# Performance work log

Measured on AMD Instinct MI355X. Metric: run time of the kernel, lower is better.

The kernel has to match this reference:

```python
import jax, jax.numpy as jnp
import numpy as np

B, H, W, C = 4, 256, 256, 16
NT = 9


def _rot2(a):
    c, s = np.cos(a), np.sin(a)
    return np.array([[c, -s], [s, c]])


def _aff(m2):
    p = np.eye(3)
    p[:2, :2] = m2
    return p


def _t(tx, ty):
    p = np.eye(3)
    p[0, 2] = tx
    p[1, 2] = ty
    return p


def _refl(direction):
    # reflection across line through origin spanned by `direction`
    v = np.asarray(direction, dtype=np.float64)
    m2 = 2.0 * np.outer(v, v) / np.dot(v, v) - np.eye(2)
    return _aff(m2)


def _get_transforms(t0, t1, t2):
    L = np.eye(3)
    L[:2, 0] = t1
    L[:2, 1] = t2
    L[:2, 2] = t0
    rot = lambda n: _aff(_rot2(2.0 * np.pi / n))
    e = np.eye(3)
    r2 = _t(.5, .5) @ rot(2) @ _t(-.5, -.5)
    r3 = _t(.5, .5) @ rot(3) @ _t(-.5, -.5)
    r4 = _t(.5, .5) @ rot(4) @ _t(-.5, -.5)
    r6 = _t(.5, .5) @ rot(6) @ _t(-.5, -.5)
    f_p = _t(0, .5) @ np.diag([1.0, -1.0, 1.0]) @ _t(0, -.5)
    f_c = np.array([[0.0, 1, 0], [1, 0, 0], [0, 0, 1]])
    f_l = _t(.5, .5) @ _refl(_rot2(5 * np.pi / 6) @ np.array([1.0, 0.0])) @ _t(-.5, -.5)
    f_s = _t(.5, .5) @ _refl(_rot2(np.pi / 3) @ np.array([1.0, 0.0])) @ _t(-.5, -.5)
    Ts = np.stack([e, r2, r3, r4, r6, f_p, f_c, f_l, f_s])
    Ts = L[None] @ Ts @ np.linalg.inv(L)[None]
    Ts = np.linalg.inv(Ts)
    Ts = Ts / Ts[:, 2:3, 2:3]  # normalize so last entry is 1
    return Ts.reshape(NT, 9)[:, :8].astype(np.float32)  # TF flat transform params


def setup_inputs() -> dict:
    key = jax.random.key(0)
    inputs = jax.random.normal(key, (B, H, W, C), dtype=jnp.float32)
    transforms = jnp.asarray(_get_transforms((0.0, 0.0), (float(H), 0.0), (0.0, float(W))))
    return {"inputs": inputs, "transforms": transforms}


def _warp_nearest(img, flat):
    # TF image_projective_transform_v2 semantics with NEAREST interpolation,
    # constant (zero) fill. flat maps OUTPUT (x,y) -> INPUT (x,y).
    b, h, w, c = img.shape
    yy, xx = jnp.meshgrid(jnp.arange(h, dtype=jnp.float32),
                          jnp.arange(w, dtype=jnp.float32), indexing="ij")
    a0, a1, a2, a3, a4, a5, a6, a7 = [flat[i] for i in range(8)]
    k = a6 * xx + a7 * yy + 1.0
    xi = jnp.round((a0 * xx + a1 * yy + a2) / k).astype(jnp.int32)
    yi = jnp.round((a3 * xx + a4 * yy + a5) / k).astype(jnp.int32)
    valid = (xi >= 0) & (xi < w) & (yi >= 0) & (yi < h)
    xi = jnp.clip(xi, 0, w - 1)
    yi = jnp.clip(yi, 0, h - 1)
    out = img[:, yi, xi, :]  # [b,h,w,c] gather
    return jnp.where(valid[None, :, :, None], out, 0.0)


def _forward(inputs, transforms):
    b, h, w, c = inputs.shape
    nt = transforms.shape[0]
    # warp the input by each of the nt group transforms: [nt,b,h,w,c]
    yw = jax.vmap(lambda m: _warp_nearest(inputs, m))(transforms)
    x = jnp.broadcast_to(inputs[None], yw.shape)
    x = jnp.transpose(x, (0, 1, 4, 2, 3))   # [nt,b,c,h,w]
    yw = jnp.transpose(yw, (0, 1, 4, 2, 3))
    # circular normalized cross-correlation via FFT, per channel image
    fx = jnp.fft.rfft2(x)
    fy = jnp.fft.rfft2(yw)
    corr = jnp.fft.irfft2(fx * jnp.conj(fy), s=(h, w))  # [nt,b,c,h,w]
    nx = jnp.linalg.norm(x.reshape(nt, b, c, -1), axis=-1)[..., None, None]
    ny = jnp.linalg.norm(yw.reshape(nt, b, c, -1), axis=-1)[..., None, None]
    corr = corr / (nx * ny + 1e-12)
    out = corr.mean(axis=2)                  # mean over channels -> [nt,b,h,w]
    return jnp.transpose(out, (1, 2, 3, 0))  # channels_last [b,h,w,nt]


def reference(inputs, transforms):
    return _forward(inputs, transforms)
```

## Files before the change

kernel.cpp:

```cpp
#include <hip/hip_runtime.h>
#include <hip/hip_fp16.h>

#define Bn  4
#define Hn  256
#define Wn  256
#define Cn  16
#define NTn 9
#define HWn (Hn*Wn)
#define KF  129
#define KGP 136
#define SRL 266
#define PI_F 3.14159265358979323846f

__device__ __forceinline__ int swz(int i) { return i ^ ((i >> 4) & 15); }

__device__ __forceinline__ float2 cmul(float2 a, float2 b) {
  float2 r = make_float2(a.x, a.x) * b;
  return r + make_float2(-a.y, a.y) * make_float2(b.y, b.x);
}

template<bool INV>
__device__ __forceinline__ void radix4(float2& x0, float2& x1, float2& x2, float2& x3) {
  float2 y0 = x0 + x2;
  float2 y1 = x0 - x2;
  float2 y2 = x1 + x3;
  float2 y3 = x1 - x3;
  float2 j3 = INV ? make_float2(-y3.y, y3.x) : make_float2(y3.y, -y3.x);
  x0 = y0 + y2;
  x2 = y0 - y2;
  x1 = y1 + j3;
  x3 = y1 - j3;
}

struct Tw { float2 a1,a2,a3,b1,b2,b3,c1,c2,c3; };

template<bool INV>
__device__ __forceinline__ Tw make_tw(int lane) {
  const float sgn = INV ? 2.0f * PI_F : -2.0f * PI_F;
  Tw t; float sw, cw;
  __sincosf(sgn * (float)lane / 256.0f, &sw, &cw);
  t.a1 = make_float2(cw, sw); t.a2 = cmul(t.a1, t.a1); t.a3 = cmul(t.a2, t.a1);
  __sincosf(sgn * (float)(lane & 15) / 64.0f, &sw, &cw);
  t.b1 = make_float2(cw, sw); t.b2 = cmul(t.b1, t.b1); t.b3 = cmul(t.b2, t.b1);
  __sincosf(sgn * (float)(lane & 3) / 16.0f, &sw, &cw);
  t.c1 = make_float2(cw, sw); t.c2 = cmul(t.c1, t.c1); t.c3 = cmul(t.c2, t.c1);
  return t;
}

template<bool INV, int NF>
__device__ __forceinline__ void fft256_n(float2 (*v)[4], float2 (*s)[SRL],
                                         int lane, const Tw& t) {
#pragma unroll
  for (int f = 0; f < NF; ++f) {
    radix4<INV>(v[f][0], v[f][1], v[f][2], v[f][3]);
    v[f][1] = cmul(v[f][1], t.a1); v[f][2] = cmul(v[f][2], t.a2); v[f][3] = cmul(v[f][3], t.a3);
#pragma unroll
    for (int a = 0; a < 4; ++a) s[f][swz(lane + (a << 6))] = v[f][a];
  }
  { int base = (lane >> 4) * 64 + (lane & 15);
#pragma unroll
    for (int f = 0; f < NF; ++f)
#pragma unroll
      for (int a = 0; a < 4; ++a) v[f][a] = s[f][swz(base + (a << 4))];
  }
#pragma unroll
  for (int f = 0; f < NF; ++f) {
    radix4<INV>(v[f][0], v[f][1], v[f][2], v[f][3]);
    v[f][1] = cmul(v[f][1], t.b1); v[f][2] = cmul(v[f][2], t.b2); v[f][3] = cmul(v[f][3], t.b3);
    int base = (lane >> 4) * 64 + (lane & 15);
#pragma unroll
    for (int a = 0; a < 4; ++a) s[f][swz(base + (a << 4))] = v[f][a];
  }
  { int base = (lane >> 4) * 64 + ((lane >> 2) & 3) * 16 + (lane & 3);
#pragma unroll
    for (int f = 0; f < NF; ++f)
#pragma unroll
      for (int a = 0; a < 4; ++a) v[f][a] = s[f][swz(base + (a << 2))];
  }
#pragma unroll
  for (int f = 0; f < NF; ++f) {
    radix4<INV>(v[f][0], v[f][1], v[f][2], v[f][3]);
    v[f][1] = cmul(v[f][1], t.c1); v[f][2] = cmul(v[f][2], t.c2); v[f][3] = cmul(v[f][3], t.c3);
    int base = (lane & ~3) * 4 + (lane & 3);
#pragma unroll
    for (int a = 0; a < 4; ++a) s[f][swz(base + (a << 2))] = v[f][a];
  }
  { int base = lane * 4;
#pragma unroll
    for (int f = 0; f < NF; ++f)
#pragma unroll
      for (int a = 0; a < 4; ++a) v[f][a] = s[f][swz(base + a)];
  }
  int dr = ((lane & 3) << 4) + (((lane >> 2) & 3) << 2) + (lane >> 4);
#pragma unroll
  for (int f = 0; f < NF; ++f) {
    radix4<INV>(v[f][0], v[f][1], v[f][2], v[f][3]);
#pragma unroll
    for (int a = 0; a < 4; ++a) s[f][swz(dr + (a << 6))] = v[f][a];
  }
}

__device__ __forceinline__ int warp_id2(float a0, float a2, float a3, float a5,
                                        float a6, float p1, float p4, float p7,
                                        bool affine, int col) {
#pragma clang fp contract(off)
  float x = (float)col;
  float xf = (a0 * x + p1) + a2;
  float yf = (a3 * x + p4) + a5;
  if (!affine) {
    float kk = (a6 * x + p7) + 1.0f;
    xf = xf / kk;
    yf = yf / kk;
  }
  float xr = rintf(xf), yr = rintf(yf);
  bool valid = (xr >= 0.f) && (xr < 256.f) && (yr >= 0.f) && (yr < 256.f);
  return valid ? ((int)yr * Wn + (int)xr) : -1;
}

__global__ __launch_bounds__(256) void k_yrow(const float* __restrict__ inp,
                                              const float* __restrict__ T,
                                              __half2* __restrict__ Yh,
                                              float* __restrict__ part) {
  __shared__ float2 sb[4][4][SRL];
  __shared__ float4 redw[4];
  int tid = threadIdx.x, w = tid >> 6, lane = tid & 63;
  Tw t = make_tw<false>(lane);
  int chunk = blockIdx.x & 15, cg = (blockIdx.x >> 4) & 3, tb = blockIdx.x >> 6;
  int b = tb & 3, tt = tb >> 2;
  int i0 = chunk << 4;
  const float4* ib = (const float4*)(inp + (size_t)b * HWn * Cn);
  float a0, a1, a2, a3, a4, a5, a6, a7;
  { const float* a = T + tt * 8;
    a0=a[0]; a1=a[1]; a2=a[2]; a3=a[3]; a4=a[4]; a5=a[5]; a6=a[6]; a7=a[7]; }
  const bool affine = (fabsf(a6) + fabsf(a7)) * 255.0f < 2.9e-8f;
  float4 nyacc = make_float4(0.f, 0.f, 0.f, 0.f);

  auto store_half = [&](int h) {
    int ii = tid & 7, kq = tid >> 3;
    int w2 = ii >> 1, odd = ii & 1;
#pragma unroll
    for (int p = 0; p < 5; ++p) {
      int k = p * 32 + kq;
      if (k <= 128) {
        int kc = (256 - k) & 255;
#pragma unroll
        for (int cc = 0; cc < 4; ++cc) {
          float2 Z  = sb[w2][cc][swz(k)];
          float2 Zc = sb[w2][cc][swz(kc)];
          float2 F = odd ? make_float2(0.5f * (Z.y + Zc.y), 0.5f * (Zc.x - Z.x))
                         : make_float2(0.5f * (Z.x + Zc.x), 0.5f * (Z.y - Zc.y));
          Yh[((size_t)(tb * Cn + cg * 4 + cc) * KF + k) * Hn + i0 + h * 8 + ii] =
              __float22half2_rn(F);
        }
      }
    }
  };

  {
    int r0 = i0 + 2 * w;
    float yA = (float)r0, yB = (float)(r0 + 1);
    float p1A = a1 * yA, p4A = a4 * yA, p7A = a7 * yA;
    float p1B = a1 * yB, p4B = a4 * yB, p7B = a7 * yB;
    float4 g0[4], g1[4];
#pragma unroll
    for (int q = 0; q < 4; ++q) {
      int col = lane + (q << 6);
      int id0 = warp_id2(a0, a2, a3, a5, a6, p1A, p4A, p7A, affine, col);
      int id1 = warp_id2(a0, a2, a3, a5, a6, p1B, p4B, p7B, affine, col);
      g0[q] = (id0 >= 0) ? ib[(size_t)id0 * 4 + cg] : make_float4(0.f,0.f,0.f,0.f);
      g1[q] = (id1 >= 0) ? ib[(size_t)id1 * 4 + cg] : make_float4(0.f,0.f,0.f,0.f);
      nyacc += g0[q] * g0[q] + g1[q] * g1[q];
    }
    float2 v[4][4];
#pragma unroll
    for (int q = 0; q < 4; ++q) {
      v[0][q] = make_float2(g0[q].x, g1[q].x);
      v[1][q] = make_float2(g0[q].y, g1[q].y);
      v[2][q] = make_float2(g0[q].z, g1[q].z);
      v[3][q] = make_float2(g0[q].w, g1[q].w);
    }
    fft256_n<false, 4>(v, sb[w], lane, t);
  }
  __syncthreads();

  float4 G0[4], G1[4];
  {
    int r1 = i0 + 8 + 2 * w;
    float yA = (float)r1, yB = (float)(r1 + 1);
    float p1A = a1 * yA, p4A = a4 * yA, p7A = a7 * yA;
    float p1B = a1 * yB, p4B = a4 * yB, p7B = a7 * yB;
#pragma unroll
    for (int q = 0; q < 4; ++q) {
      int col = lane + (q << 6);
      int id0 = warp_id2(a0, a2, a3, a5, a6, p1A, p4A, p7A, affine, col);
      int id1 = warp_id2(a0, a2, a3, a5, a6, p1B, p4B, p7B, affine, col);
      G0[q] = (id0 >= 0) ? ib[(size_t)id0 * 4 + cg] : make_float4(0.f,0.f,0.f,0.f);
      G1[q] = (id1 >= 0) ? ib[(size_t)id1 * 4 + cg] : make_float4(0.f,0.f,0.f,0.f);
    }
  }

  store_half(0);
  __syncthreads();

  {
#pragma unroll
    for (int q = 0; q < 4; ++q)
      nyacc += G0[q] * G0[q] + G1[q] * G1[q];
    float2 v[4][4];
#pragma unroll
    for (int q = 0; q < 4; ++q) {
      v[0][q] = make_float2(G0[q].x, G1[q].x);
      v[1][q] = make_float2(G0[q].y, G1[q].y);
      v[2][q] = make_float2(G0[q].z, G1[q].z);
      v[3][q] = make_float2(G0[q].w, G1[q].w);
    }
    fft256_n<false, 4>(v, sb[w], lane, t);
  }
  __syncthreads();
  store_half(1);

#pragma unroll
  for (int o = 32; o > 0; o >>= 1) {
    nyacc.x += __shfl_down(nyacc.x, o, 64);
    nyacc.y += __shfl_down(nyacc.y, o, 64);
    nyacc.z += __shfl_down(nyacc.z, o, 64);
    nyacc.w += __shfl_down(nyacc.w, o, 64);
  }
  if (lane == 0) redw[w] = nyacc;
  __syncthreads();
  if (tid == 0) {
    float4 s = make_float4(redw[0].x + redw[1].x + redw[2].x + redw[3].x,
                           redw[0].y + redw[1].y + redw[2].y + redw[3].y,
                           redw[0].z + redw[1].z + redw[2].z + redw[3].z,
                           redw[0].w + redw[1].w + redw[2].w + redw[3].w);
    part[((size_t)tb * Cn + cg * 4 + 0) * 16 + chunk] = s.x;
    part[((size_t)tb * Cn + cg * 4 + 1) * 16 + chunk] = s.y;
    part[((size_t)tb * Cn + cg * 4 + 2) * 16 + chunk] = s.z;
    part[((size_t)tb * Cn + cg * 4 + 3) * 16 + chunk] = s.w;
  }
}

__global__ __launch_bounds__(256) void k_colfft_fx(const __half2* __restrict__ Yh,
                                                   __half2* __restrict__ Fxh) {
  __shared__ float2 sb[4][4][SRL];
  int tid = threadIdx.x, w = tid >> 6, lane = tid & 63;
  Tw t = make_tw<false>(lane);
  int base_item = blockIdx.x * 16 + w * 4;
  float2 v[4][4];
#pragma unroll
  for (int f = 0; f < 4; ++f) {
    const __half2* Sp = Yh + (size_t)(base_item + f) * Hn;
#pragma unroll
    for (int q = 0; q < 4; ++q) v[f][q] = __half22float2(Sp[lane + (q << 6)]);
  }
  fft256_n<false, 4>(v, sb[w], lane, t);
#pragma unroll
  for (int f = 0; f < 4; ++f) {
    __half2* Op = Fxh + (size_t)(base_item + f) * Hn;
#pragma unroll
    for (int q = 0; q < 4; ++q) {
      int j = lane + (q << 6);
      Op[j] = __float22half2_rn(sb[w][f][swz(j)]);
    }
  }
}

__global__ __launch_bounds__(256) void k_ycol(const __half2* __restrict__ Yh,
                                              const __half2* __restrict__ Fxh,
                                              const float* __restrict__ part,
                                              float2* __restrict__ G) {
  __shared__ float2 sb[4][4][SRL];
  __shared__ float scs[16];
  int tid = threadIdx.x, w = tid >> 6, lane = tid & 63;
  int tb = blockIdx.x / 33, quart = blockIdx.x % 33;
  int b = tb & 3;
  if (tid < 16) {
    float sx = 0.f, sy = 0.f;
#pragma unroll
    for (int ch = 0; ch < 16; ++ch) {
      sx += part[((size_t)b  * Cn + tid) * 16 + ch];
      sy += part[((size_t)tb * Cn + tid) * 16 + ch];
    }
    scs[tid] = 1.0f / ((float)Cn * (sqrtf(sx) * sqrtf(sy) + 1e-12f));
  }
  __syncthreads();
  int k = quart * 4 + w;
  bool act = (k <= 128);
  if (act) {
    Tw tf = make_tw<false>(lane);
    float2 acc[4];
#pragma unroll
    for (int q = 0; q < 4; ++q) acc[q] = make_float2(0.f, 0.f);
    const __half2* Ybase = Yh  + ((size_t)(tb * Cn) * KF + k) * Hn;
    const __half2* Fbase = Fxh + ((size_t)(b  * Cn) * KF + k) * Hn;

    float2 va[4][4], vb[4][4];
    auto LOADY = [&](float2 (*v)[4], int c0) {
#pragma unroll
      for (int e = 0; e < 4; ++e) {
        const __half2* Yp = Ybase + (size_t)(c0 + e) * KF * Hn;
#pragma unroll
        for (int q = 0; q < 4; ++q) v[e][q] = __half22float2(Yp[lane + (q << 6)]);
      }
    };
    auto ACC = [&](int c0) {
#pragma unroll
      for (int e = 0; e < 4; ++e) {
        float sc = scs[c0 + e];
        const __half2* Fxp = Fbase + (size_t)(c0 + e) * KF * Hn;
#pragma unroll
        for (int q = 0; q < 4; ++q) {
          int rr = lane + (q << 6);
          float2 fy = sb[w][e][swz(rr)];
          float2 fx = __half22float2(Fxp[rr]);
          float2 pr = make_float2(fy.x, fy.x) * fx
                    + make_float2(fy.y, fy.y) * make_float2(fx.y, -fx.x);
          acc[q] += make_float2(sc, sc) * pr;
        }
      }
    };

    LOADY(va, 0);
    fft256_n<false, 4>(va, sb[w], lane, tf);  LOADY(vb, 4);   ACC(0);
    fft256_n<false, 4>(vb, sb[w], lane, tf);  LOADY(va, 8);   ACC(4);
    fft256_n<false, 4>(va, sb[w], lane, tf);  LOADY(vb, 12);  ACC(8);
    fft256_n<false, 4>(vb, sb[w], lane, tf);                  ACC(12);

    Tw ti = make_tw<true>(lane);
    fft256_n<true, 1>(reinterpret_cast<float2(*)[4]>(acc), sb[w], lane, ti);
  }
  __syncthreads();
  int kk = tid & 3, jj0 = tid >> 2;
  if (quart * 4 + kk <= 128) {
    float2* Gp = G + ((size_t)tb * Hn) * KGP + quart * 4 + kk;
#pragma unroll
    for (int p = 0; p < 4; ++p) {
      int j = jj0 + (p << 6);
      Gp[(size_t)j * KGP] = sb[kk][0][swz(j)];
    }
  }
}

__global__ __launch_bounds__(320) void k_irow(const float2* __restrict__ G,
                                              float* __restrict__ out) {
  __shared__ float2 tile[5][2][132];
  __shared__ float2 sb[5][SRL];
  __shared__ float rowbuf[Wn * NTn];
  int tid = threadIdx.x, w = tid >> 6, lane = tid & 63;
  Tw ti = make_tw<true>(lane);
  int b = blockIdx.x >> 8, i = blockIdx.x & 255;
  const float scale = 1.0f / ((float)Hn * (float)Wn);
  int t1 = 2 * w, t2 = t1 + 1;
  {
    const float2* Gp1 = G + ((size_t)(t1 * Bn + b) * Hn + i) * KGP;
    for (int k = lane; k < KF; k += 64) tile[w][0][k] = Gp1[k];
    if (t2 < NTn) {
      const float2* Gp2 = G + ((size_t)(t2 * Bn + b) * Hn + i) * KGP;
      for (int k = lane; k < KF; k += 64) tile[w][1][k] = Gp2[k];
    }
  }
  float2 v[1][4];
#pragma unroll
  for (int q = 0; q < 4; ++q) {
    int k = lane + (q << 6);
    float2 a, bb;
    if (k <= 128) a = tile[w][0][k];
    else { float2 z = tile[w][0][256 - k]; a = make_float2(z.x, -z.y); }
    if (t2 < NTn) {
      if (k <= 128) bb = tile[w][1][k];
      else { float2 z = tile[w][1][256 - k]; bb = make_float2(z.x, -z.y); }
    } else bb = make_float2(0.f, 0.f);
    v[0][q] = a + make_float2(-bb.y, bb.x);
  }
  fft256_n<true, 1>(v, reinterpret_cast<float2(*)[SRL]>(sb[w]), lane, ti);
#pragma unroll
  for (int q = 0; q < 4; ++q) {
    int j = lane + (q << 6);
    float2 r = sb[w][swz(j)];
    rowbuf[j * NTn + t1] = r.x * scale;
    if (t2 < NTn) rowbuf[j * NTn + t2] = r.y * scale;
  }
  __syncthreads();
  float* ob = out + ((size_t)(b * Hn + i) * Wn) * NTn;
  for (int f = tid; f < Wn * NTn; f += 320) ob[f] = rowbuf[f];
}

extern "C" void kernel_launch(void* const* d_in, const int* in_sizes, int n_in,
                              void* d_out, int out_size, void* d_ws, size_t ws_size,
                              hipStream_t stream) {
  const float* inp = (const float*)d_in[0];
  const float* T   = (const float*)d_in[1];
  float* out = (float*)d_out;
  char* ws = (char*)d_ws;

  size_t off = 0;
  float*   part = (float*)(ws + off);  off += (size_t)NTn * Bn * Cn * 16 * sizeof(float);
  __half2* Fxh = (__half2*)(ws + off); off += (size_t)Bn * Cn * KF * Hn * sizeof(__half2);
  float2*  G   = (float2*)(ws + off);  off += (size_t)NTn * Bn * Hn * KGP * sizeof(float2);
  __half2* Yh  = (__half2*)(ws + off); off += (size_t)NTn * Bn * Cn * KF * Hn * sizeof(__half2);
  (void)off; (void)ws_size; (void)in_sizes; (void)n_in; (void)out_size;

  k_yrow<<<NTn * Bn * 64, 256, 0, stream>>>(inp, T, Yh, part);
  k_colfft_fx<<<Bn * Cn * KF / 4 / 4, 256, 0, stream>>>(Yh, Fxh);
  k_ycol<<<NTn * Bn * 33, 256, 0, stream>>>(Yh, Fxh, part, G);
  k_irow<<<Bn * Hn, 320, 0, stream>>>(G, out);
}
```

Baseline: 178.0 us.

## Process all channel groups per block in k_yrow, reusing warp indices

Each k_yrow block now handles all four channel groups instead of one, and the grid shrinks to a quarter of its former size. The warped source indices are computed once per block and reused across the groups, which removes redundant index math (including perspective divides). Gathers for the next FFT stage are issued alongside stores of the previous stage in a software-pipelined sequence. In exchange the grid drops to 576 blocks, which lowers occupancy and parallelism, and each block has a longer serial chain of syncs and more live registers.

```diff
diff --git a/kernel.cpp b/kernel.cpp
--- a/kernel.cpp
+++ b/kernel.cpp
@@ -122,10 +122,10 @@
                                               __half2* __restrict__ Yh,
                                               float* __restrict__ part) {
   __shared__ float2 sb[4][4][SRL];
-  __shared__ float4 redw[4];
+  __shared__ float4 redw[4][4];
   int tid = threadIdx.x, w = tid >> 6, lane = tid & 63;
   Tw t = make_tw<false>(lane);
-  int chunk = blockIdx.x & 15, cg = (blockIdx.x >> 4) & 3, tb = blockIdx.x >> 6;
+  int chunk = blockIdx.x & 15, tb = blockIdx.x >> 4;
   int b = tb & 3, tt = tb >> 2;
   int i0 = chunk << 4;
   const float4* ib = (const float4*)(inp + (size_t)b * HWn * Cn);
@@ -133,9 +133,48 @@
   { const float* a = T + tt * 8;
     a0=a[0]; a1=a[1]; a2=a[2]; a3=a[3]; a4=a[4]; a5=a[5]; a6=a[6]; a7=a[7]; }
   const bool affine = (fabsf(a6) + fabsf(a7)) * 255.0f < 2.9e-8f;
-  float4 nyacc = make_float4(0.f, 0.f, 0.f, 0.f);
-
-  auto store_half = [&](int h) {
+
+  int id[2][2][4];
+#pragma unroll
+  for (int h = 0; h < 2; ++h) {
+    int r0 = i0 + h * 8 + 2 * w;
+    float yA = (float)r0, yB = (float)(r0 + 1);
+    float p1A = a1 * yA, p4A = a4 * yA, p7A = a7 * yA;
+    float p1B = a1 * yB, p4B = a4 * yB, p7B = a7 * yB;
+#pragma unroll
+    for (int q = 0; q < 4; ++q) {
+      int col = lane + (q << 6);
+      int i0_ = warp_id2(a0, a2, a3, a5, a6, p1A, p4A, p7A, affine, col);
+      int i1_ = warp_id2(a0, a2, a3, a5, a6, p1B, p4B, p7B, affine, col);
+      id[h][0][q] = (i0_ >= 0) ? i0_ * 4 : -1;
+      id[h][1][q] = (i1_ >= 0) ? i1_ * 4 : -1;
+    }
+  }
+
+  float4 ny0 = make_float4(0.f,0.f,0.f,0.f), ny1 = ny0, ny2 = ny0, ny3 = ny0;
+  float4 gA0[4], gA1[4], gB0[4], gB1[4];
+
+  auto GATHER = [&](float4* g0, float4* g1, int h, int cg) {
+#pragma unroll
+    for (int q = 0; q < 4; ++q) {
+      int a0i = id[h][0][q], a1i = id[h][1][q];
+      g0[q] = (a0i >= 0) ? ib[a0i + cg] : make_float4(0.f,0.f,0.f,0.f);
+      g1[q] = (a1i >= 0) ? ib[a1i + cg] : make_float4(0.f,0.f,0.f,0.f);
+    }
+  };
+  auto FFT_CONSUME = [&](float4* g0, float4* g1, float4& ny) {
+    float2 v[4][4];
+#pragma unroll
+    for (int q = 0; q < 4; ++q) {
+      ny += g0[q] * g0[q] + g1[q] * g1[q];
+      v[0][q] = make_float2(g0[q].x, g1[q].x);
+      v[1][q] = make_float2(g0[q].y, g1[q].y);
+      v[2][q] = make_float2(g0[q].z, g1[q].z);
+      v[3][q] = make_float2(g0[q].w, g1[q].w);
+    }
+    fft256_n<false, 4>(v, sb[w], lane, t);
+  };
+  auto store_half = [&](int cg, int h) {
     int ii = tid & 7, kq = tid >> 3;
     int w2 = ii >> 1, odd = ii & 1;
 #pragma unroll
@@ -156,87 +195,54 @@
     }
   };
 
-  {
-    int r0 = i0 + 2 * w;
-    float yA = (float)r0, yB = (float)(r0 + 1);
-    float p1A = a1 * yA, p4A = a4 * yA, p7A = a7 * yA;
-    float p1B = a1 * yB, p4B = a4 * yB, p7B = a7 * yB;
-    float4 g0[4], g1[4];
-#pragma unroll
-    for (int q = 0; q < 4; ++q) {
-      int col = lane + (q << 6);
-      int id0 = warp_id2(a0, a2, a3, a5, a6, p1A, p4A, p7A, affine, col);
-      int id1 = warp_id2(a0, a2, a3, a5, a6, p1B, p4B, p7B, affine, col);
-      g0[q] = (id0 >= 0) ? ib[(size_t)id0 * 4 + cg] : make_float4(0.f,0.f,0.f,0.f);
-      g1[q] = (id1 >= 0) ? ib[(size_t)id1 * 4 + cg] : make_float4(0.f,0.f,0.f,0.f);
-      nyacc += g0[q] * g0[q] + g1[q] * g1[q];
-    }
-    float2 v[4][4];
-#pragma unroll
-    for (int q = 0; q < 4; ++q) {
-      v[0][q] = make_float2(g0[q].x, g1[q].x);
-      v[1][q] = make_float2(g0[q].y, g1[q].y);
-      v[2][q] = make_float2(g0[q].z, g1[q].z);
-      v[3][q] = make_float2(g0[q].w, g1[q].w);
-    }
-    fft256_n<false, 4>(v, sb[w], lane, t);
-  }
-  __syncthreads();
-
-  float4 G0[4], G1[4];
-  {
-    int r1 = i0 + 8 + 2 * w;
-    float yA = (float)r1, yB = (float)(r1 + 1);
-    float p1A = a1 * yA, p4A = a4 * yA, p7A = a7 * yA;
-    float p1B = a1 * yB, p4B = a4 * yB, p7B = a7 * yB;
-#pragma unroll
-    for (int q = 0; q < 4; ++q) {
-      int col = lane + (q << 6);
-      int id0 = warp_id2(a0, a2, a3, a5, a6, p1A, p4A, p7A, affine, col);
-      int id1 = warp_id2(a0, a2, a3, a5, a6, p1B, p4B, p7B, affine, col);
-      G0[q] = (id0 >= 0) ? ib[(size_t)id0 * 4 + cg] : make_float4(0.f,0.f,0.f,0.f);
-      G1[q] = (id1 >= 0) ? ib[(size_t)id1 * 4 + cg] : make_float4(0.f,0.f,0.f,0.f);
-    }
-  }
-
-  store_half(0);
-  __syncthreads();
-
-  {
-#pragma unroll
-    for (int q = 0; q < 4; ++q)
-      nyacc += G0[q] * G0[q] + G1[q] * G1[q];
-    float2 v[4][4];
-#pragma unroll
-    for (int q = 0; q < 4; ++q) {
-      v[0][q] = make_float2(G0[q].x, G1[q].x);
-      v[1][q] = make_float2(G0[q].y, G1[q].y);
-      v[2][q] = make_float2(G0[q].z, G1[q].z);
-      v[3][q] = make_float2(G0[q].w, G1[q].w);
-    }
-    fft256_n<false, 4>(v, sb[w], lane, t);
-  }
-  __syncthreads();
-  store_half(1);
+  GATHER(gA0, gA1, 0, 0);
+  FFT_CONSUME(gA0, gA1, ny0);
+  __syncthreads();
+  GATHER(gB0, gB1, 1, 0);  store_half(0, 0);  __syncthreads();
+  FFT_CONSUME(gB0, gB1, ny0);
+  __syncthreads();
+  GATHER(gA0, gA1, 0, 1);  store_half(0, 1);  __syncthreads();
+  FFT_CONSUME(gA0, gA1, ny1);
+  __syncthreads();
+  GATHER(gB0, gB1, 1, 1);  store_half(1, 0);  __syncthreads();
+  FFT_CONSUME(gB0, gB1, ny1);
+  __syncthreads();
+  GATHER(gA0, gA1, 0, 2);  store_half(1, 1);  __syncthreads();
+  FFT_CONSUME(gA0, gA1, ny2);
+  __syncthreads();
+  GATHER(gB0, gB1, 1, 2);  store_half(2, 0);  __syncthreads();
+  FFT_CONSUME(gB0, gB1, ny2);
+  __syncthreads();
+  GATHER(gA0, gA1, 0, 3);  store_half(2, 1);  __syncthreads();
+  FFT_CONSUME(gA0, gA1, ny3);
+  __syncthreads();
+  GATHER(gB0, gB1, 1, 3);  store_half(3, 0);  __syncthreads();
+  FFT_CONSUME(gB0, gB1, ny3);
+  __syncthreads();
+  store_half(3, 1);
 
 #pragma unroll
   for (int o = 32; o > 0; o >>= 1) {
-    nyacc.x += __shfl_down(nyacc.x, o, 64);
-    nyacc.y += __shfl_down(nyacc.y, o, 64);
-    nyacc.z += __shfl_down(nyacc.z, o, 64);
-    nyacc.w += __shfl_down(nyacc.w, o, 64);
-  }
-  if (lane == 0) redw[w] = nyacc;
+    ny0.x += __shfl_down(ny0.x, o, 64); ny0.y += __shfl_down(ny0.y, o, 64);
+    ny0.z += __shfl_down(ny0.z, o, 64); ny0.w += __shfl_down(ny0.w, o, 64);
+    ny1.x += __shfl_down(ny1.x, o, 64); ny1.y += __shfl_down(ny1.y, o, 64);
+    ny1.z += __shfl_down(ny1.z, o, 64); ny1.w += __shfl_down(ny1.w, o, 64);
+    ny2.x += __shfl_down(ny2.x, o, 64); ny2.y += __shfl_down(ny2.y, o, 64);
+    ny2.z += __shfl_down(ny2.z, o, 64); ny2.w += __shfl_down(ny2.w, o, 64);
+    ny3.x += __shfl_down(ny3.x, o, 64); ny3.y += __shfl_down(ny3.y, o, 64);
+    ny3.z += __shfl_down(ny3.z, o, 64); ny3.w += __shfl_down(ny3.w, o, 64);
+  }
+  if (lane == 0) { redw[w][0] = ny0; redw[w][1] = ny1; redw[w][2] = ny2; redw[w][3] = ny3; }
   __syncthreads();
   if (tid == 0) {
-    float4 s = make_float4(redw[0].x + redw[1].x + redw[2].x + redw[3].x,
-                           redw[0].y + redw[1].y + redw[2].y + redw[3].y,
-                           redw[0].z + redw[1].z + redw[2].z + redw[3].z,
-                           redw[0].w + redw[1].w + redw[2].w + redw[3].w);
-    part[((size_t)tb * Cn + cg * 4 + 0) * 16 + chunk] = s.x;
-    part[((size_t)tb * Cn + cg * 4 + 1) * 16 + chunk] = s.y;
-    part[((size_t)tb * Cn + cg * 4 + 2) * 16 + chunk] = s.z;
-    part[((size_t)tb * Cn + cg * 4 + 3) * 16 + chunk] = s.w;
+#pragma unroll
+    for (int cg = 0; cg < 4; ++cg) {
+      float4 s = redw[0][cg] + redw[1][cg] + redw[2][cg] + redw[3][cg];
+      part[((size_t)tb * Cn + cg * 4 + 0) * 16 + chunk] = s.x;
+      part[((size_t)tb * Cn + cg * 4 + 1) * 16 + chunk] = s.y;
+      part[((size_t)tb * Cn + cg * 4 + 2) * 16 + chunk] = s.z;
+      part[((size_t)tb * Cn + cg * 4 + 3) * 16 + chunk] = s.w;
+    }
   }
 }
 
@@ -400,7 +406,7 @@
   __half2* Yh  = (__half2*)(ws + off); off += (size_t)NTn * Bn * Cn * KF * Hn * sizeof(__half2);
   (void)off; (void)ws_size; (void)in_sizes; (void)n_in; (void)out_size;
 
-  k_yrow<<<NTn * Bn * 64, 256, 0, stream>>>(inp, T, Yh, part);
+  k_yrow<<<NTn * Bn * 16, 256, 0, stream>>>(inp, T, Yh, part);
   k_colfft_fx<<<Bn * Cn * KF / 4 / 4, 256, 0, stream>>>(Yh, Fxh);
   k_ycol<<<NTn * Bn * 33, 256, 0, stream>>>(Yh, Fxh, part, G);
   k_irow<<<Bn * Hn, 320, 0, stream>>>(G, out);
```

Measured after the change: 242.5 us. 1.36x slower.
